# Optimization experiments

Measured on AMD Instinct MI355X. Metric: run time of the kernel, lower is better.

## Reference

```python
import math
import jax, jax.numpy as jnp
import numpy as np

B, T, S = 4, 4096, 1024
HID, CTX, EMB, H = 1024, 768, 1024, 16
D = EMB // H  # head_dim = 64


def setup_inputs() -> dict:
    key = jax.random.key(0)
    ks = jax.random.split(key, 7)
    sc = lambda n: 1.0 / math.sqrt(n)
    return {
        "tokens": jax.random.normal(ks[0], (B, T, HID), jnp.float32),
        "context": jax.random.normal(ks[1], (B, S, CTX), jnp.float32),
        "Wq": jax.random.normal(ks[2], (HID, EMB), jnp.float32) * sc(HID),
        "Wk": jax.random.normal(ks[3], (CTX, EMB), jnp.float32) * sc(CTX),
        "Wv": jax.random.normal(ks[4], (CTX, EMB), jnp.float32) * sc(CTX),
        "Wo": jax.random.normal(ks[5], (EMB, HID), jnp.float32) * sc(EMB),
        "bo": jnp.zeros((HID,), jnp.float32),
    }


def reference(tokens, context, Wq, Wk, Wv, Wo, bo):
    # projections (bias-free, as in torch Linear(bias=False))
    Q = tokens @ Wq              # [B,T,EMB]
    K = context @ Wk             # [B,S,EMB]
    V = context @ Wv             # [B,S,EMB]
    # split heads: B T (H D) -> B H T D
    Q = Q.reshape(B, T, H, D).transpose(0, 2, 1, 3)
    K = K.reshape(B, S, H, D).transpose(0, 2, 1, 3)
    V = V.reshape(B, S, H, D).transpose(0, 2, 1, 3)
    scores = jnp.einsum('bhtd,bhsd->bhts', Q, K) / math.sqrt(D)
    attn = jax.nn.softmax(scores, axis=-1)
    ctx = jnp.einsum('bhts,bhsd->bhtd', attn, V)
    ctx = ctx.transpose(0, 2, 1, 3).reshape(B, T, EMB)
    return ctx @ Wo + bo
```

## Files before the change

### kernel.cpp

```cpp
#include <hip/hip_runtime.h>
#include <hip/hip_bf16.h>

#define B_ 4
#define T_ 4096
#define S_ 1024
#define HID_ 1024
#define CTX_ 768
#define EMB_ 1024
#define H_ 16
#define D_ 64

#define QSCALE 0.18033688011112042f

typedef __attribute__((ext_vector_type(8))) short short8;
typedef __attribute__((ext_vector_type(4))) float f32x4;
typedef __attribute__((ext_vector_type(4))) unsigned short us4;
typedef unsigned short ushort_t;

__device__ inline ushort_t f2b(float f) {
  union { float f; unsigned u; } x; x.f = f;
  return (ushort_t)((x.u + 0x7fffu + ((x.u >> 16) & 1u)) >> 16);
}
__device__ inline unsigned cvtpk2(float a, float b) {
  __hip_bfloat162 h = __float22bfloat162_rn(float2{a, b});
  union { __hip_bfloat162 h; unsigned u; } c; c.h = h; return c.u;
}
__device__ inline ushort_t f2b_fast(float f) {
  __hip_bfloat16 h = __float2bfloat16(f);
  union { __hip_bfloat16 h; ushort_t u; } c; c.h = h; return c.u;
}

using gu32p = const __attribute__((address_space(1))) unsigned int*;
using lu32p = __attribute__((address_space(3))) unsigned int*;
__device__ inline void gload16(const ushort_t* g, ushort_t* l) {
  __builtin_amdgcn_global_load_lds((gu32p)(const void*)g, (lu32p)(void*)l, 16, 0, 0);
}

__device__ inline void conv_body(const float* __restrict__ in, ushort_t* __restrict__ out,
                                 int blk, int tid) {
  const size_t i = ((size_t)blk * 256 + tid) * 8;
  const float4 a = *(const float4*)(in + i);
  const float4 b = *(const float4*)(in + i + 4);
  uint4 u;
  u.x = cvtpk2(a.x, a.y); u.y = cvtpk2(a.z, a.w);
  u.z = cvtpk2(b.x, b.y); u.w = cvtpk2(b.z, b.w);
  *(uint4*)(out + i) = u;
}

__device__ inline void convT_body(const float* __restrict__ W, ushort_t* __restrict__ Wt,
                                  int K, int tile, int tid, float (*Ls)[33]) {
  const int n0 = (tile & 31) * 32, k0 = (tile >> 5) * 32;
  const int r = tid >> 3, c4 = (tid & 7) * 4;
  const float4 v = *(const float4*)&W[(size_t)(k0 + r) * 1024 + n0 + c4];
  Ls[r][c4] = v.x; Ls[r][c4 + 1] = v.y; Ls[r][c4 + 2] = v.z; Ls[r][c4 + 3] = v.w;
  __syncthreads();
  us4 o;
  o.x = f2b_fast(Ls[c4][r]);     o.y = f2b_fast(Ls[c4 + 1][r]);
  o.z = f2b_fast(Ls[c4 + 2][r]); o.w = f2b_fast(Ls[c4 + 3][r]);
  *(us4*)&Wt[(size_t)(n0 + r) * K + k0 + c4] = o;
}

__global__ __launch_bounds__(256) void prepA(
    const float* __restrict__ context,
    const float* __restrict__ Wq, const float* __restrict__ Wk,
    const float* __restrict__ Wv,
    ushort_t* __restrict__ CtxB, ushort_t* __restrict__ WqT,
    ushort_t* __restrict__ WkvT)
{
  __shared__ float Ls[32][33];
  const int tid = threadIdx.x;
  int blk = (int)blockIdx.x;
  if (blk < 1536) { conv_body(context, CtxB, blk, tid); return; }
  blk -= 1536;
  if (blk < 1024) { convT_body(Wq, WqT, 1024, blk, tid, Ls); return; }
  blk -= 1024;
  if (blk < 768)  { convT_body(Wk, WkvT, 768, blk, tid, Ls); return; }
  blk -= 768;
  convT_body(Wv, WkvT + (size_t)1024 * 768, 768, blk, tid, Ls);
}

__global__ __launch_bounds__(256) void prepO(const float* __restrict__ Wo,
                                             ushort_t* __restrict__ WoT) {
  __shared__ float Ls[32][33];
  convT_body(Wo, WoT, 1024, (int)blockIdx.x, threadIdx.x, Ls);
}

__global__ __launch_bounds__(512) void gemm256kv(
    const ushort_t* __restrict__ A, const ushort_t* __restrict__ Bt,
    ushort_t* __restrict__ Kb, ushort_t* __restrict__ Vtb)
{
  constexpr int Kd = CTX_, NT = CTX_ / 32;
  extern __shared__ ushort_t L[];
  const int tid = threadIdx.x;
  const int lane = tid & 63, wid = tid >> 6;
  const int lr = lane & 15, lg = lane >> 4;
  const int wm = wid >> 2, wn = wid & 3;

  const int lin = (int)blockIdx.x;
  const int swz = (lin & 7) * 32 + (lin >> 3);
  const int bm = swz >> 3, bn = swz & 7;

  const int sr = tid >> 2;
  const int csrc = (tid & 3) ^ ((sr >> 1) & 3);
  const ushort_t* gA = A + (size_t)(bm * 128 + sr) * Kd + csrc * 8;
  const ushort_t* gB = Bt + (size_t)(bn * 256 + sr) * Kd + csrc * 8;
  const size_t halfB = (size_t)128 * Kd;

  f32x4 acc[4][4] = {};

#define KVSTAGE(c, slot) do { const int k0_ = (c) << 5;            \
    ushort_t* s_ = L + (slot) * 12288;                             \
    gload16(gA + k0_, s_ + tid * 8);                               \
    gload16(gB + k0_, s_ + 4096 + tid * 8);                        \
    gload16(gB + k0_ + halfB, s_ + 8192 + tid * 8);                \
  } while (0)

  KVSTAGE(0, 0); KVSTAGE(1, 1);
  int cur = 0, sls = 2;
  for (int t = 0; t < NT; ++t) {
    if (t < NT - 1) asm volatile("s_waitcnt vmcnt(3)" ::: "memory");
    else            asm volatile("s_waitcnt vmcnt(0)" ::: "memory");
    __builtin_amdgcn_s_barrier();
    __builtin_amdgcn_sched_barrier(0);
    if (t + 2 < NT) KVSTAGE(t + 2, sls);
    const ushort_t* As_ = L + cur * 12288;
    const ushort_t* Bs_ = As_ + 4096;
    short8 af[4], bf[4];
#pragma unroll
    for (int m = 0; m < 4; ++m) {
      const int row = wm * 64 + m * 16 + lr;
      af[m] = *(const short8*)&As_[row * 32 + (lg ^ ((row >> 1) & 3)) * 8];
    }
#pragma unroll
    for (int n = 0; n < 4; ++n) {
      const int row = wn * 64 + n * 16 + lr;
      bf[n] = *(const short8*)&Bs_[row * 32 + (lg ^ ((row >> 1) & 3)) * 8];
    }
    __builtin_amdgcn_s_setprio(1);
#pragma unroll
    for (int m = 0; m < 4; ++m)
#pragma unroll
      for (int n = 0; n < 4; ++n)
        acc[m][n] = __builtin_amdgcn_mfma_f32_16x16x32_bf16(af[m], bf[n], acc[m][n], 0, 0, 0);
    __builtin_amdgcn_s_setprio(0);
    cur = (cur == 2) ? 0 : cur + 1;
    sls = (sls == 2) ? 0 : sls + 1;
  }
#undef KVSTAGE

  const int row0 = bm * 128 + wm * 64 + lg * 4;
  const int col0 = bn * 256 + wn * 64 + lr;

  if (col0 < 1024) {
#pragma unroll
    for (int m = 0; m < 4; ++m)
#pragma unroll
      for (int n = 0; n < 4; ++n) {
        const int col = col0 + n * 16;
#pragma unroll
        for (int i = 0; i < 4; ++i)
          Kb[(size_t)(row0 + m * 16 + i) * EMB_ + col] = f2b_fast(acc[m][n][i]);
      }
  } else {
#pragma unroll
    for (int m = 0; m < 4; ++m) {
      const int rbase = row0 + m * 16;
      const int bb = rbase >> 10;
      const int s0 = rbase & (S_ - 1);
#pragma unroll
      for (int n = 0; n < 4; ++n) {
        const int vc = col0 + n * 16 - 1024;
        const int hh = vc >> 6, dd = vc & 63;
        us4 o;
        o.x = f2b_fast(acc[m][n][0]); o.y = f2b_fast(acc[m][n][1]);
        o.z = f2b_fast(acc[m][n][2]); o.w = f2b_fast(acc[m][n][3]);
        *(us4*)&Vtb[(((size_t)bb * H_ + hh) * D_ + dd) * S_ + s0] = o;
      }
    }
  }
}

template<int EPI>
__global__ __launch_bounds__(512) void gemm256(
    const ushort_t* __restrict__ A, const ushort_t* __restrict__ Bt,
    void* __restrict__ Cp, const float* __restrict__ bias,
    int M, int Kd, int N)
{
  extern __shared__ ushort_t L[];
  const int tid = threadIdx.x;
  const int lane = tid & 63, wid = tid >> 6;
  const int lr = lane & 15, lg = lane >> 4;
  const int wm = wid >> 2, wn = wid & 3;

  const int cpx = (int)gridDim.x >> 3;
  const int lin = (int)blockIdx.x;
  const int swz = (lin & 7) * cpx + (lin >> 3);
  const int nbn = N >> 8;
  const int bm = swz / nbn, bn = swz % nbn;

  const int sr = tid >> 2;
  const int csrc = (tid & 3) ^ ((sr >> 1) & 3);
  const ushort_t* gA = A + (size_t)(bm * 256 + sr) * Kd + csrc * 8;
  const ushort_t* gB = Bt + (size_t)(bn * 256 + sr) * Kd + csrc * 8;
  const size_t half = (size_t)128 * Kd;
  ushort_t* const dA = L + tid * 8;
  ushort_t* const dB = L + 8192 + tid * 8;

  f32x4 acc[8][4] = {};
  const int NT = Kd >> 5;

#define STAGE256(c) do {                                \
    const int slot_ = ((c) & 3) * 16384;                \
    const int k0_ = (c) << 5;                           \
    gload16(gA + k0_, dA + slot_);                      \
    gload16(gA + k0_ + half, dA + slot_ + 4096);        \
    gload16(gB + k0_, dB + slot_);                      \
    gload16(gB + k0_ + half, dB + slot_ + 4096);        \
  } while (0)

  STAGE256(0); STAGE256(1); STAGE256(2);
  asm volatile("s_waitcnt vmcnt(8)" ::: "memory");
  __builtin_amdgcn_s_barrier();
  __builtin_amdgcn_sched_barrier(0);

  for (int t = 0; t < NT; ++t) {
    if (t + 3 < NT) STAGE256(t + 3);
    const ushort_t* As_ = L + (t & 3) * 16384;
    const ushort_t* Bs_ = As_ + 8192;
    short8 af[8], bf[4];
#pragma unroll
    for (int m = 0; m < 8; ++m) {
      const int row = wm * 128 + m * 16 + lr;
      af[m] = *(const short8*)&As_[row * 32 + (lg ^ ((row >> 1) & 3)) * 8];
    }
#pragma unroll
    for (int n = 0; n < 4; ++n) {
      const int row = wn * 64 + n * 16 + lr;
      bf[n] = *(const short8*)&Bs_[row * 32 + (lg ^ ((row >> 1) & 3)) * 8];
    }
    __builtin_amdgcn_s_setprio(1);
#pragma unroll
    for (int m = 0; m < 8; ++m)
#pragma unroll
      for (int n = 0; n < 4; ++n)
        acc[m][n] = __builtin_amdgcn_mfma_f32_16x16x32_bf16(af[m], bf[n], acc[m][n], 0, 0, 0);
    __builtin_amdgcn_s_setprio(0);
    asm volatile("s_waitcnt vmcnt(8)" ::: "memory");
    __builtin_amdgcn_s_barrier();
    __builtin_amdgcn_sched_barrier(0);
  }
#undef STAGE256

  const int row0 = bm * 256 + wm * 128 + lg * 4;
  const int col0 = bn * 256 + wn * 64 + lr;

  if constexpr (EPI == 3) {
    float* C = (float*)Cp;
#pragma unroll
    for (int n = 0; n < 4; ++n) {
      const int col = col0 + n * 16;
      const float bv = bias[col];
#pragma unroll
      for (int m = 0; m < 8; ++m)
#pragma unroll
        for (int i = 0; i < 4; ++i)
          C[(size_t)(row0 + m * 16 + i) * N + col] = acc[m][n][i] + bv;
    }
  } else {
    ushort_t* C = (ushort_t*)Cp;
#pragma unroll
    for (int m = 0; m < 8; ++m)
#pragma unroll
      for (int n = 0; n < 4; ++n) {
        const int col = col0 + n * 16;
#pragma unroll
        for (int i = 0; i < 4; ++i)
          C[(size_t)(row0 + m * 16 + i) * N + col] = f2b(acc[m][n][i] * QSCALE);
      }
  }
}

__global__ __launch_bounds__(512) void gemm256f(
    const float* __restrict__ Af, const ushort_t* __restrict__ Bt,
    ushort_t* __restrict__ Cp, int M, int N)
{
  constexpr int Kd = 1024, NT = 32;
  extern __shared__ ushort_t L[];
  const int tid = threadIdx.x;
  const int lane = tid & 63, wid = tid >> 6;
  const int lr = lane & 15, lg = lane >> 4;
  const int wm = wid >> 2, wn = wid & 3;

  const int cpx = (int)gridDim.x >> 3;
  const int lin = (int)blockIdx.x;
  const int swz = (lin & 7) * cpx + (lin >> 3);
  const int nbn = N >> 8;
  const int bm = swz / nbn, bn = swz % nbn;

  const int sr = tid >> 2;
  const int csrc = (tid & 3) ^ ((sr >> 1) & 3);
  const float* gA = Af + (size_t)(bm * 256 + sr) * Kd + csrc * 8;
  const ushort_t* gB = Bt + (size_t)(bn * 256 + sr) * Kd + csrc * 8;
  const size_t half = (size_t)128 * Kd;
  ushort_t* const dA = L + tid * 8;
  ushort_t* const dB = L + 8192 + tid * 8;

  f32x4 acc[8][4] = {};
  float4 ra0[4], ra1[4];

#define ALOADF(c, RS) do { const int k0_ = (c) << 5;      \
    RS[0] = *(const float4*)(gA + k0_);                   \
    RS[1] = *(const float4*)(gA + k0_ + 4);               \
    RS[2] = *(const float4*)(gA + k0_ + half);            \
    RS[3] = *(const float4*)(gA + k0_ + half + 4);        \
  } while (0)

#define AWRITE(c, RS) do { const int slot_ = ((c) & 3) * 16384;  \
    uint4 u0, u1;                                                \
    u0.x = cvtpk2(RS[0].x, RS[0].y); u0.y = cvtpk2(RS[0].z, RS[0].w); \
    u0.z = cvtpk2(RS[1].x, RS[1].y); u0.w = cvtpk2(RS[1].z, RS[1].w); \
    u1.x = cvtpk2(RS[2].x, RS[2].y); u1.y = cvtpk2(RS[2].z, RS[2].w); \
    u1.z = cvtpk2(RS[3].x, RS[3].y); u1.w = cvtpk2(RS[3].z, RS[3].w); \
    *(uint4*)(dA + slot_) = u0;                                  \
    *(uint4*)(dA + slot_ + 4096) = u1;                           \
  } while (0)

#define BSTAGE(c) do { const int slot_ = ((c) & 3) * 16384; const int k0_ = (c) << 5; \
    gload16(gB + k0_, dB + slot_);                      \
    gload16(gB + k0_ + half, dB + slot_ + 4096);        \
  } while (0)

#define COMPUTE(c) do {                                                  \
    const ushort_t* As_ = L + ((c) & 3) * 16384;                         \
    const ushort_t* Bs_ = As_ + 8192;                                    \
    short8 af[8], bf[4];                                                 \
    _Pragma("unroll")                                                    \
    for (int m = 0; m < 8; ++m) {                                        \
      const int row = wm * 128 + m * 16 + lr;                            \
      af[m] = *(const short8*)&As_[row * 32 + (lg ^ ((row >> 1) & 3)) * 8]; \
    }                                                                    \
    _Pragma("unroll")                                                    \
    for (int n = 0; n < 4; ++n) {                                        \
      const int row = wn * 64 + n * 16 + lr;                             \
      bf[n] = *(const short8*)&Bs_[row * 32 + (lg ^ ((row >> 1) & 3)) * 8]; \
    }                                                                    \
    __builtin_amdgcn_s_setprio(1);                                       \
    _Pragma("unroll")                                                    \
    for (int m = 0; m < 8; ++m)                                          \
      _Pragma("unroll")                                                  \
      for (int n = 0; n < 4; ++n)                                        \
        acc[m][n] = __builtin_amdgcn_mfma_f32_16x16x32_bf16(af[m], bf[n], acc[m][n], 0, 0, 0); \
    __builtin_amdgcn_s_setprio(0);                                       \
  } while (0)

#define ENDBAR do {                                        \
    asm volatile("s_waitcnt lgkmcnt(0)" ::: "memory");     \
    __builtin_amdgcn_s_barrier();                          \
    __builtin_amdgcn_sched_barrier(0);                     \
  } while (0)

  {
    float4 p0[4], p1[4], p2[4];
    ALOADF(0, p0); ALOADF(1, p1); ALOADF(2, p2);
    AWRITE(0, p0); AWRITE(1, p1); AWRITE(2, p2);
    BSTAGE(0); BSTAGE(1); BSTAGE(2);
    ALOADF(3, ra1);
    asm volatile("s_waitcnt vmcnt(4)" ::: "memory");
    ENDBAR;
  }

  for (int t = 0; t < NT; t += 2) {
    if (t + 3 < NT) { AWRITE(t + 3, ra1); BSTAGE(t + 3); }
    if (t + 4 < NT) ALOADF(t + 4, ra0);
    COMPUTE(t);
    ENDBAR;
    if (t + 4 < NT) { AWRITE(t + 4, ra0); BSTAGE(t + 4); }
    if (t + 5 < NT) ALOADF(t + 5, ra1);
    COMPUTE(t + 1);
    ENDBAR;
  }
#undef ALOADF
#undef AWRITE
#undef BSTAGE
#undef COMPUTE
#undef ENDBAR

  const int row0 = bm * 256 + wm * 128 + lg * 4;
  const int col0 = bn * 256 + wn * 64 + lr;
#pragma unroll
  for (int m = 0; m < 8; ++m)
#pragma unroll
    for (int n = 0; n < 4; ++n) {
      const int col = col0 + n * 16;
#pragma unroll
      for (int i = 0; i < 4; ++i)
        Cp[(size_t)(row0 + m * 16 + i) * N + col] = f2b(acc[m][n][i] * QSCALE);
    }
}

__global__ __launch_bounds__(512) void attn_v8(
    const ushort_t* __restrict__ Q, const ushort_t* __restrict__ K,
    const ushort_t* __restrict__ Vt, ushort_t* __restrict__ C)
{
  extern __shared__ ushort_t SM[];
  const int tid = threadIdx.x;
  const int lane = tid & 63, w = tid >> 6;
  const int lr = lane & 15, lg = lane >> 4;

  const int bid = (int)blockIdx.x;
  const int g = (bid & 7) | (((bid >> 3) >> 4) << 3);
  const int tb = (bid >> 3) & 15;
  const int h = g & 15, b = g >> 4;
  const int t0 = tb * 256;

  short8 qf[2][2];
#pragma unroll
  for (int qs = 0; qs < 2; ++qs) {
    const size_t qrow = (size_t)b * T_ + t0 + w * 32 + qs * 16 + lr;
    const ushort_t* qp = Q + qrow * EMB_ + h * 64;
    qf[qs][0] = *(const short8*)(qp + lg * 8);
    qf[qs][1] = *(const short8*)(qp + 32 + lg * 8);
  }

  short8 ones;
#pragma unroll
  for (int j = 0; j < 8; ++j) ones[j] = (short)0x3F80;

  f32x4 o[2][4] = {};
  f32x4 lacc[2] = {};

  const int srow = tid >> 3, schunk = tid & 7;
  const int sswz = schunk ^ (srow & 7);
  const ushort_t* kg = K + ((size_t)b * S_ + srow) * EMB_ + h * 64 + sswz * 8;
  const ushort_t* vg = Vt + (((size_t)b * H_ + h) * D_ + srow) * S_ + sswz * 8;
  ushort_t* Psw = SM + 24576 + w * 1152;

  gload16(kg, SM + tid * 8);
  gload16(vg, SM + 12288 + tid * 8);
  gload16(kg + (size_t)64 * EMB_, SM + 4096 + tid * 8);
  gload16(vg + 64, SM + 12288 + 4096 + tid * 8);

  int cur = 0, sls = 2;
  for (int st = 0; st < 16; ++st) {
    if (st < 15) asm volatile("s_waitcnt vmcnt(2)" ::: "memory");
    else         asm volatile("s_waitcnt vmcnt(0)" ::: "memory");
    __builtin_amdgcn_s_barrier();
    __builtin_amdgcn_sched_barrier(0);
    if (st + 2 < 16) {
      gload16(kg + (size_t)(st + 2) * 64 * EMB_, SM + sls * 4096 + tid * 8);
      gload16(vg + (st + 2) * 64, SM + 12288 + sls * 4096 + tid * 8);
    }
    const ushort_t* Ksb = SM + cur * 4096;
    const ushort_t* Vsb = SM + 12288 + cur * 4096;

    f32x4 sacc[2][4] = {};
    __builtin_amdgcn_s_setprio(1);
#pragma unroll
    for (int c = 0; c < 4; ++c) {
      const int krow = c * 16 + lr;
      const int sw = krow & 7;
      const short8 ka0 = *(const short8*)&Ksb[krow * 64 + ((lg ^ sw) * 8)];
      const short8 ka1 = *(const short8*)&Ksb[krow * 64 + (((4 + lg) ^ sw) * 8)];
#pragma unroll
      for (int qs = 0; qs < 2; ++qs) {
        sacc[qs][c] = __builtin_amdgcn_mfma_f32_16x16x32_bf16(ka0, qf[qs][0], sacc[qs][c], 0, 0, 0);
        sacc[qs][c] = __builtin_amdgcn_mfma_f32_16x16x32_bf16(ka1, qf[qs][1], sacc[qs][c], 0, 0, 0);
      }
    }
    __builtin_amdgcn_s_setprio(0);

    short8 pa[2][2];
#pragma unroll
    for (int qs = 0; qs < 2; ++qs) {
#pragma unroll
      for (int c = 0; c < 4; ++c) {
        uint2 pk;
        pk.x = cvtpk2(exp2f(sacc[qs][c][0]), exp2f(sacc[qs][c][1]));
        pk.y = cvtpk2(exp2f(sacc[qs][c][2]), exp2f(sacc[qs][c][3]));
        *(uint2*)&Psw[lr * 72 + c * 16 + lg * 4] = pk;
      }
      pa[qs][0] = *(const short8*)&Psw[lr * 72 + lg * 8];
      pa[qs][1] = *(const short8*)&Psw[lr * 72 + 32 + lg * 8];
    }

    __builtin_amdgcn_s_setprio(1);
#pragma unroll
    for (int sh = 0; sh < 2; ++sh) {
#pragma unroll
      for (int dc = 0; dc < 4; ++dc) {
        const int vrow = dc * 16 + lr;
        const int vsw = vrow & 7;
        const short8 vb = *(const short8*)&Vsb[vrow * 64 + (((sh * 4 + lg) ^ vsw) * 8)];
        o[0][dc] = __builtin_amdgcn_mfma_f32_16x16x32_bf16(pa[0][sh], vb, o[0][dc], 0, 0, 0);
        o[1][dc] = __builtin_amdgcn_mfma_f32_16x16x32_bf16(pa[1][sh], vb, o[1][dc], 0, 0, 0);
      }
      lacc[0] = __builtin_amdgcn_mfma_f32_16x16x32_bf16(pa[0][sh], ones, lacc[0], 0, 0, 0);
      lacc[1] = __builtin_amdgcn_mfma_f32_16x16x32_bf16(pa[1][sh], ones, lacc[1], 0, 0, 0);
    }
    __builtin_amdgcn_s_setprio(0);

    cur = (cur == 2) ? 0 : cur + 1;
    sls = (sls == 2) ? 0 : sls + 1;
  }

#pragma unroll
  for (int qs = 0; qs < 2; ++qs) {
#pragma unroll
    for (int i = 0; i < 4; ++i) {
      const float li = 1.0f / lacc[qs][i];
      const size_t trow = (size_t)b * T_ + t0 + w * 32 + qs * 16 + lg * 4 + i;
#pragma unroll
      for (int dc = 0; dc < 4; ++dc)
        C[trow * EMB_ + h * 64 + dc * 16 + lr] = f2b_fast(o[qs][dc][i] * li);
    }
  }
}

extern "C" void kernel_launch(void* const* d_in, const int* in_sizes, int n_in,
                              void* d_out, int out_size, void* d_ws, size_t ws_size,
                              hipStream_t stream) {
  const float* tokens  = (const float*)d_in[0];
  const float* context = (const float*)d_in[1];
  const float* Wq = (const float*)d_in[2];
  const float* Wk = (const float*)d_in[3];
  const float* Wv = (const float*)d_in[4];
  const float* Wo = (const float*)d_in[5];
  const float* bo = (const float*)d_in[6];
  float* out = (float*)d_out;

  ushort_t* Qb  = (ushort_t*)d_out;
  ushort_t* Kb   = (ushort_t*)d_ws;
  ushort_t* Vtb  = Kb + (size_t)B_ * S_ * EMB_;
  ushort_t* Cb   = Vtb + (size_t)B_ * S_ * EMB_;
  ushort_t* WqT  = Cb + (size_t)B_ * T_ * EMB_;
  ushort_t* WkvT = WqT + (size_t)EMB_ * HID_;

  prepA<<<4096, 256, 0, stream>>>(context, Wq, Wk, Wv, Cb, WqT, WkvT);
  gemm256f<<<dim3((B_ * T_ / 256) * (EMB_ / 256)), 512, 131072, stream>>>(
      tokens, WqT, Qb, B_ * T_, EMB_);
  prepO<<<1024, 256, 0, stream>>>(Wo, WqT);
  gemm256kv<<<dim3(256), 512, 73728, stream>>>(Cb, WkvT, Kb, Vtb);
  attn_v8<<<dim3((T_ / 256) * H_ * B_), 512, 67584, stream>>>(Qb, Kb, Vtb, Cb);
  gemm256<3><<<dim3((B_ * T_ / 256) * (HID_ / 256)), 512, 131072, stream>>>(
      Cb, WqT, out, bo, B_ * T_, EMB_, HID_);
}
```

Baseline: 226.9 us.

## Fuse Wo transpose into prep kernel and interleave output GEMM loads

The Wo transpose-convert moves into the prepA kernel and writes to its own WoT buffer, which removes one kernel launch. The output projection GEMM is rewritten with a 3-slot LDS ring instead of 4 slots, lowering shared memory from 128KB to 96KB. Each k-step is split into four quarters, and each quarter issues one async global load alongside its MFMA group, with extra barriers between quarters. The aim is finer-grained overlap of loads and compute and possibly higher occupancy, at the cost of more barrier synchronisation per iteration.

Result: no change. 224.9 us (-0.9%).

```diff
diff --git a/kernel.cpp b/kernel.cpp
--- a/kernel.cpp
+++ b/kernel.cpp
@@ -63,9 +63,9 @@
 __global__ __launch_bounds__(256) void prepA(
     const float* __restrict__ context,
     const float* __restrict__ Wq, const float* __restrict__ Wk,
-    const float* __restrict__ Wv,
+    const float* __restrict__ Wv, const float* __restrict__ Wo,
     ushort_t* __restrict__ CtxB, ushort_t* __restrict__ WqT,
-    ushort_t* __restrict__ WkvT)
+    ushort_t* __restrict__ WkvT, ushort_t* __restrict__ WoT)
 {
   __shared__ float Ls[32][33];
   const int tid = threadIdx.x;
@@ -76,13 +76,9 @@
   blk -= 1024;
   if (blk < 768)  { convT_body(Wk, WkvT, 768, blk, tid, Ls); return; }
   blk -= 768;
-  convT_body(Wv, WkvT + (size_t)1024 * 768, 768, blk, tid, Ls);
-}
-
-__global__ __launch_bounds__(256) void prepO(const float* __restrict__ Wo,
-                                             ushort_t* __restrict__ WoT) {
-  __shared__ float Ls[32][33];
-  convT_body(Wo, WoT, 1024, (int)blockIdx.x, threadIdx.x, Ls);
+  if (blk < 768)  { convT_body(Wv, WkvT + (size_t)1024 * 768, 768, blk, tid, Ls); return; }
+  blk -= 768;
+  convT_body(Wo, WoT, 1024, blk, tid, Ls);
 }
 
 __global__ __launch_bounds__(512) void gemm256kv(
@@ -180,10 +176,9 @@
   }
 }
 
-template<int EPI>
-__global__ __launch_bounds__(512) void gemm256(
+__global__ __launch_bounds__(512) void gemm256p(
     const ushort_t* __restrict__ A, const ushort_t* __restrict__ Bt,
-    void* __restrict__ Cp, const float* __restrict__ bias,
+    float* __restrict__ Cp, const float* __restrict__ bias,
     int M, int Kd, int N)
 {
   extern __shared__ ushort_t L[];
@@ -203,80 +198,78 @@
   const ushort_t* gA = A + (size_t)(bm * 256 + sr) * Kd + csrc * 8;
   const ushort_t* gB = Bt + (size_t)(bn * 256 + sr) * Kd + csrc * 8;
   const size_t half = (size_t)128 * Kd;
-  ushort_t* const dA = L + tid * 8;
-  ushort_t* const dB = L + 8192 + tid * 8;
 
   f32x4 acc[8][4] = {};
   const int NT = Kd >> 5;
 
-#define STAGE256(c) do {                                \
-    const int slot_ = ((c) & 3) * 16384;                \
-    const int k0_ = (c) << 5;                           \
-    gload16(gA + k0_, dA + slot_);                      \
-    gload16(gA + k0_ + half, dA + slot_ + 4096);        \
-    gload16(gB + k0_, dB + slot_);                      \
-    gload16(gB + k0_ + half, dB + slot_ + 4096);        \
-  } while (0)
-
-  STAGE256(0); STAGE256(1); STAGE256(2);
-  asm volatile("s_waitcnt vmcnt(8)" ::: "memory");
+#define STAGEQ(c, q) do {                                            \
+    const int k0_ = (c) << 5;                                        \
+    ushort_t* s_ = L + ((c) % 3) * 16384 + (q) * 4096 + tid * 8;     \
+    if ((q) == 0)      gload16(gA + k0_, s_);                        \
+    else if ((q) == 1) gload16(gA + k0_ + half, s_);                 \
+    else if ((q) == 2) gload16(gB + k0_, s_);                        \
+    else               gload16(gB + k0_ + half, s_);                 \
+  } while (0)
+
+#pragma unroll
+  for (int q = 0; q < 4; ++q) STAGEQ(0, q);
+#pragma unroll
+  for (int q = 0; q < 4; ++q) STAGEQ(1, q);
+  asm volatile("s_waitcnt vmcnt(4)" ::: "memory");
   __builtin_amdgcn_s_barrier();
   __builtin_amdgcn_sched_barrier(0);
 
   for (int t = 0; t < NT; ++t) {
-    if (t + 3 < NT) STAGE256(t + 3);
-    const ushort_t* As_ = L + (t & 3) * 16384;
+    const ushort_t* As_ = L + (t % 3) * 16384;
     const ushort_t* Bs_ = As_ + 8192;
-    short8 af[8], bf[4];
-#pragma unroll
-    for (int m = 0; m < 8; ++m) {
-      const int row = wm * 128 + m * 16 + lr;
-      af[m] = *(const short8*)&As_[row * 32 + (lg ^ ((row >> 1) & 3)) * 8];
-    }
-#pragma unroll
-    for (int n = 0; n < 4; ++n) {
-      const int row = wn * 64 + n * 16 + lr;
-      bf[n] = *(const short8*)&Bs_[row * 32 + (lg ^ ((row >> 1) & 3)) * 8];
-    }
-    __builtin_amdgcn_s_setprio(1);
-#pragma unroll
-    for (int m = 0; m < 8; ++m)
+    const bool st = (t + 2 < NT);
+    short8 bf[4];
+#pragma unroll
+    for (int q = 0; q < 4; ++q) {
+      if (q == 0) {
+#pragma unroll
+        for (int n = 0; n < 4; ++n) {
+          const int row = wn * 64 + n * 16 + lr;
+          bf[n] = *(const short8*)&Bs_[row * 32 + (lg ^ ((row >> 1) & 3)) * 8];
+        }
+      }
+      const int r0 = wm * 128 + (2 * q) * 16 + lr;
+      const int r1 = r0 + 16;
+      const short8 af0 = *(const short8*)&As_[r0 * 32 + (lg ^ ((r0 >> 1) & 3)) * 8];
+      const short8 af1 = *(const short8*)&As_[r1 * 32 + (lg ^ ((r1 >> 1) & 3)) * 8];
+      if (st) STAGEQ(t + 2, q);
+      __builtin_amdgcn_s_barrier();
+      asm volatile("s_waitcnt lgkmcnt(0)" ::: "memory");
+      __builtin_amdgcn_sched_barrier(0);
+      __builtin_amdgcn_s_setprio(1);
 #pragma unroll
       for (int n = 0; n < 4; ++n)
-        acc[m][n] = __builtin_amdgcn_mfma_f32_16x16x32_bf16(af[m], bf[n], acc[m][n], 0, 0, 0);
-    __builtin_amdgcn_s_setprio(0);
-    asm volatile("s_waitcnt vmcnt(8)" ::: "memory");
-    __builtin_amdgcn_s_barrier();
-    __builtin_amdgcn_sched_barrier(0);
-  }
-#undef STAGE256
+        acc[2 * q][n] = __builtin_amdgcn_mfma_f32_16x16x32_bf16(af0, bf[n], acc[2 * q][n], 0, 0, 0);
+#pragma unroll
+      for (int n = 0; n < 4; ++n)
+        acc[2 * q + 1][n] = __builtin_amdgcn_mfma_f32_16x16x32_bf16(af1, bf[n], acc[2 * q + 1][n], 0, 0, 0);
+      __builtin_amdgcn_s_setprio(0);
+      if (q == 3 && t < NT - 1) {
+        if (st) asm volatile("s_waitcnt vmcnt(4)" ::: "memory");
+        else    asm volatile("s_waitcnt vmcnt(0)" ::: "memory");
+      }
+      __builtin_amdgcn_s_barrier();
+      __builtin_amdgcn_sched_barrier(0);
+    }
+  }
+#undef STAGEQ
 
   const int row0 = bm * 256 + wm * 128 + lg * 4;
   const int col0 = bn * 256 + wn * 64 + lr;
-
-  if constexpr (EPI == 3) {
-    float* C = (float*)Cp;
-#pragma unroll
-    for (int n = 0; n < 4; ++n) {
-      const int col = col0 + n * 16;
-      const float bv = bias[col];
-#pragma unroll
-      for (int m = 0; m < 8; ++m)
-#pragma unroll
-        for (int i = 0; i < 4; ++i)
-          C[(size_t)(row0 + m * 16 + i) * N + col] = acc[m][n][i] + bv;
-    }
-  } else {
-    ushort_t* C = (ushort_t*)Cp;
+#pragma unroll
+  for (int n = 0; n < 4; ++n) {
+    const int col = col0 + n * 16;
+    const float bv = bias[col];
 #pragma unroll
     for (int m = 0; m < 8; ++m)
 #pragma unroll
-      for (int n = 0; n < 4; ++n) {
-        const int col = col0 + n * 16;
-#pragma unroll
-        for (int i = 0; i < 4; ++i)
-          C[(size_t)(row0 + m * 16 + i) * N + col] = f2b(acc[m][n][i] * QSCALE);
-      }
+      for (int i = 0; i < 4; ++i)
+        Cp[(size_t)(row0 + m * 16 + i) * N + col] = acc[m][n][i] + bv;
   }
 }
 
@@ -534,13 +527,13 @@
   ushort_t* Cb   = Vtb + (size_t)B_ * S_ * EMB_;
   ushort_t* WqT  = Cb + (size_t)B_ * T_ * EMB_;
   ushort_t* WkvT = WqT + (size_t)EMB_ * HID_;
-
-  prepA<<<4096, 256, 0, stream>>>(context, Wq, Wk, Wv, Cb, WqT, WkvT);
+  ushort_t* WoT  = WkvT + (size_t)EMB_ * 2 * CTX_;
+
+  prepA<<<5120, 256, 0, stream>>>(context, Wq, Wk, Wv, Wo, Cb, WqT, WkvT, WoT);
   gemm256f<<<dim3((B_ * T_ / 256) * (EMB_ / 256)), 512, 131072, stream>>>(
       tokens, WqT, Qb, B_ * T_, EMB_);
-  prepO<<<1024, 256, 0, stream>>>(Wo, WqT);
   gemm256kv<<<dim3(256), 512, 73728, stream>>>(Cb, WkvT, Kb, Vtb);
   attn_v8<<<dim3((T_ / 256) * H_ * B_), 512, 67584, stream>>>(Qb, Kb, Vtb, Cb);
-  gemm256<3><<<dim3((B_ * T_ / 256) * (HID_ / 256)), 512, 131072, stream>>>(
-      Cb, WqT, out, bo, B_ * T_, EMB_, HID_);
-}
+  gemm256p<<<dim3((B_ * T_ / 256) * (HID_ / 256)), 512, 98304, stream>>>(
+      Cb, WoT, out, bo, B_ * T_, EMB_, HID_);
+}
```
